# Kernel tuning notes

Measured on AMD Instinct MI355X. Metric: run time of the kernel, lower is better.

The kernel has to match this reference:

```python
import jax, jax.numpy as jnp
import numpy as np

D_MODEL = 256
D_STATE = 16
D_CONV = 4
DT_RANK = 16  # ceil(d_model/16)


def _silu(v):
    return v * jax.nn.sigmoid(v)


def _mamba(x, in_w, cw, cb, xp_w, dt_w, dt_b, A_log, Dp, out_w):
    """One Mamba head (d_inner == d_model since expand=1). x: (B, L, D)."""
    B, L, D = x.shape
    xz = x @ in_w.T                       # (B, L, 2D)
    xc, z = jnp.split(xz, 2, axis=-1)
    # causal depthwise conv1d, kernel D_CONV
    xpad = jnp.pad(xc, ((0, 0), (D_CONV - 1, 0), (0, 0)))
    conv = cb + sum(xpad[:, k:k + L, :] * cw[:, k] for k in range(D_CONV))
    xc = _silu(conv)
    dbl = xc @ xp_w.T                     # (B, L, dt_rank + 2N)
    dt_r = dbl[..., :DT_RANK]
    Bm = dbl[..., DT_RANK:DT_RANK + D_STATE]      # (B, L, N)
    Cm = dbl[..., DT_RANK + D_STATE:]             # (B, L, N)
    dt = jax.nn.softplus(dt_r @ dt_w.T + dt_b)    # (B, L, D)
    A = -jnp.exp(A_log)                            # (D, N)
    dA = jnp.exp(dt[..., None] * A)                # (B, L, D, N)
    dBx = (dt * xc)[..., None] * Bm[:, :, None, :] # (B, L, D, N)

    def step(h, inp):
        a, b = inp
        h = a * h + b
        return h, h

    h0 = jnp.zeros((B, D, D_STATE), x.dtype)
    _, hs = jax.lax.scan(step, h0, (jnp.moveaxis(dA, 1, 0), jnp.moveaxis(dBx, 1, 0)))
    y = jnp.einsum('lbdn,bln->bld', hs, Cm) + Dp * xc
    y = y * _silu(z)
    return y @ out_w.T


def setup_inputs() -> dict:
    key = jax.random.key(0)
    ks = jax.random.split(key, 8)
    D, N, R = D_MODEL, D_STATE, DT_RANK
    B, H, W = 4, 32, 32
    s = 0.02
    x = jax.random.normal(ks[0], (B, D, H, W), jnp.float32)
    in_proj_w = jax.random.normal(ks[1], (4, 2 * D, D), jnp.float32) * s
    conv_w = jax.random.normal(ks[2], (4, D, D_CONV), jnp.float32) * 0.1
    conv_b = jax.random.normal(ks[3], (4, D), jnp.float32) * 0.02
    x_proj_w = jax.random.normal(ks[4], (4, R + 2 * N, D), jnp.float32) * s
    dt_w = jax.random.normal(ks[5], (4, D, R), jnp.float32) * s
    dt_b = jax.random.normal(ks[6], (4, D), jnp.float32) * 0.02
    A_log = jnp.tile(jnp.log(jnp.arange(1, N + 1, dtype=jnp.float32)), (4, D, 1))
    D_skip = jnp.ones((4, D), jnp.float32)
    out_proj_w = jax.random.normal(ks[7], (4, D, D), jnp.float32) * s
    scale_mod = jnp.ones((1,), jnp.float32) * 0.25
    return {"x": x, "in_proj_w": in_proj_w, "conv_w": conv_w, "conv_b": conv_b,
            "x_proj_w": x_proj_w, "dt_w": dt_w, "dt_b": dt_b, "A_log": A_log,
            "D_skip": D_skip, "out_proj_w": out_proj_w, "scale_mod": scale_mod}


def reference(x, in_proj_w, conv_w, conv_b, x_proj_w, dt_w, dt_b, A_log, D_skip, out_proj_w, scale_mod):
    B, C, H, W = x.shape
    x_flat = x.transpose(0, 2, 3, 1).reshape(B, H * W, C)       # row-major scan order
    x_v = x_flat.reshape(B, H, W, C).transpose(0, 2, 1, 3).reshape(B, H * W, C)  # column-major
    inp4 = jnp.stack([x_flat, x_flat[:, ::-1], x_v, x_v[:, ::-1]])  # (4, B, L, C)
    outs = jax.vmap(_mamba)(inp4, in_proj_w, conv_w, conv_b, x_proj_w,
                            dt_w, dt_b, A_log, D_skip, out_proj_w)
    o0 = outs[0]
    o1 = outs[1][:, ::-1]
    o2 = outs[2].reshape(B, W, H, C).transpose(0, 2, 1, 3).reshape(B, H * W, C)
    o3 = outs[3][:, ::-1].reshape(B, W, H, C).transpose(0, 2, 1, 3).reshape(B, H * W, C)
    return (o0 + o1 + o2 + o3) / 4 * scale_mod
```

## Files before the change

### kernel.cpp

```cpp
#include <hip/hip_runtime.h>
#include <cstddef>

#define NDIR 4
#define NB 4
#define DM 256
#define NS 16
#define LL 1024
#define TCH 32
#define NCHUNK 32

typedef __attribute__((ext_vector_type(8))) short bf16x8;
typedef __attribute__((ext_vector_type(4))) float f32x4;

__device__ __forceinline__ float silu_f(float v) { return v / (1.0f + __expf(-v)); }
__device__ __forceinline__ float softplus_f(float v) {
    return fmaxf(v, 0.0f) + __logf(1.0f + __expf(-fabsf(v)));
}

__device__ __forceinline__ short bf16_hi(float v, float& vh) {
    unsigned u = __float_as_uint(v);
    unsigned r = (u + 0x7FFFu + ((u >> 16) & 1u)) & 0xFFFF0000u;
    vh = __uint_as_float(r);
    return (short)(r >> 16);
}
__device__ __forceinline__ short bf16_rn(float v) {
    unsigned u = __float_as_uint(v);
    return (short)((u + 0x7FFFu + ((u >> 16) & 1u)) >> 16);
}
__device__ __forceinline__ float bf16_to_f(short s) {
    return __uint_as_float(((unsigned)(unsigned short)s) << 16);
}

__device__ __forceinline__ int lmap(int dir, int l) {
    int lt = (dir & 2) ? (((l & 31) << 5) | (l >> 5)) : l;
    return (dir & 1) ? (1023 - lt) : lt;
}

__global__ __launch_bounds__(256) void k0w_prep(const float* __restrict__ x,
                                                const float* __restrict__ in_w,
                                                const float* __restrict__ xp_w,
                                                const float* __restrict__ out_w,
                                                short* __restrict__ Ah,
                                                short* __restrict__ Al,
                                                short* __restrict__ wh,
                                                short* __restrict__ wl) {
    int bid = blockIdx.x;
    int tid = threadIdx.x;
    if (bid < 1024) {
        int b  = bid & 3;
        int c0 = ((bid >> 2) & 7) << 5;
        int hh = (bid >> 5) & 31;
        __shared__ float T[32][33];
        int w  = tid & 31;
        int cl = tid >> 5;
#pragma unroll
        for (int it = 0; it < 4; ++it) {
            int c = cl + (it << 3);
            T[c][w] = x[(((size_t)(b << 8) + c0 + c) << 10) + (hh << 5) + w];
        }
        __syncthreads();
        int co = tid & 31;
        int wl_ = tid >> 5;
#pragma unroll
        for (int it = 0; it < 4; ++it) {
            int wo = wl_ + (it << 3);
            float v = T[co][wo];
            float vh;
            short hs = bf16_hi(v, vh);
            short ls = bf16_rn(v - vh);
            size_t idx = (((size_t)(b << 10) + (hh << 5) + wo) << 8) + c0 + co;
            Ah[idx] = hs;
            Al[idx] = ls;
        }
    } else {
        int t = ((bid - 1024) << 8) + tid;
        const float* src;
        size_t e;
        if (t < 131072)      { src = in_w  + ((size_t)t << 2);            e = (size_t)t << 2; }
        else if (t < 143360) { src = xp_w  + ((size_t)(t - 131072) << 2); e = 524288 + ((size_t)(t - 131072) << 2); }
        else                 { src = out_w + ((size_t)(t - 143360) << 2); e = 573440 + ((size_t)(t - 143360) << 2); }
        float4 v = *(const float4*)src;
        short4 H, L;
        float vh;
        H.x = bf16_hi(v.x, vh); L.x = bf16_rn(v.x - vh);
        H.y = bf16_hi(v.y, vh); L.y = bf16_rn(v.y - vh);
        H.z = bf16_hi(v.z, vh); L.z = bf16_rn(v.z - vh);
        H.w = bf16_hi(v.w, vh); L.w = bf16_rn(v.w - vh);
        *(short4*)(wh + e) = H;
        *(short4*)(wl + e) = L;
    }
}

__global__ __launch_bounds__(256, 2) void k1_mfma(const short* __restrict__ Ah,
                                                  const short* __restrict__ Al,
                                                  const short* __restrict__ Bh,
                                                  const short* __restrict__ Bl,
                                                  float* __restrict__ xzc,
                                                  float* __restrict__ xzz) {
    __shared__ short sAh[8192], sAl[8192], sBh[8192], sBl[8192];
    int mt = blockIdx.x, nt = blockIdx.y;
    int tid = threadIdx.x;
    int wv = tid >> 6, lane = tid & 63;
    int wm = wv >> 1, wn = wv & 1;
    int lrow = lane & 15, lk = lane >> 4;
    f32x4 acc[4][4] = {};
    int sr[4], sg[4], soff[4];
#pragma unroll
    for (int i = 0; i < 4; ++i) {
        int slot = (i << 8) + tid;
        sr[i] = slot >> 3; sg[i] = slot & 7;
        soff[i] = (sr[i] << 6) + ((sg[i] ^ (sr[i] & 7)) << 3);
    }
    bf16x8 vah[4], val_[4], vbh[4], vbl[4];
#define K1_LOAD(KK) do { \
    int k0_ = (KK) << 6; \
    _Pragma("unroll") \
    for (int i = 0; i < 4; ++i) { \
        size_t ao = (size_t)((mt << 7) + sr[i]) * 256 + k0_ + (sg[i] << 3); \
        size_t bo = (size_t)((nt << 7) + sr[i]) * 256 + k0_ + (sg[i] << 3); \
        vah[i]  = *(const bf16x8*)(Ah + ao); \
        val_[i] = *(const bf16x8*)(Al + ao); \
        vbh[i]  = *(const bf16x8*)(Bh + bo); \
        vbl[i]  = *(const bf16x8*)(Bl + bo); \
    } } while (0)
    K1_LOAD(0);
    for (int kk = 0; kk < 4; ++kk) {
        if (kk) __syncthreads();
#pragma unroll
        for (int i = 0; i < 4; ++i) {
            *(bf16x8*)&sAh[soff[i]] = vah[i];
            *(bf16x8*)&sAl[soff[i]] = val_[i];
            *(bf16x8*)&sBh[soff[i]] = vbh[i];
            *(bf16x8*)&sBl[soff[i]] = vbl[i];
        }
        __syncthreads();
        if (kk < 3) K1_LOAD(kk + 1);
#pragma unroll
        for (int kh = 0; kh < 2; ++kh) {
            int g = (kh << 2) + lk;
            bf16x8 ah[4], al[4], bh[4], bl[4];
#pragma unroll
            for (int m = 0; m < 4; ++m) {
                int r = (wm << 6) + (m << 4) + lrow;
                int off = (r << 6) + ((g ^ (r & 7)) << 3);
                ah[m] = *(const bf16x8*)&sAh[off];
                al[m] = *(const bf16x8*)&sAl[off];
            }
#pragma unroll
            for (int n = 0; n < 4; ++n) {
                int r = (wn << 6) + (n << 4) + lrow;
                int off = (r << 6) + ((g ^ (r & 7)) << 3);
                bh[n] = *(const bf16x8*)&sBh[off];
                bl[n] = *(const bf16x8*)&sBl[off];
            }
#pragma unroll
            for (int m = 0; m < 4; ++m)
#pragma unroll
                for (int n = 0; n < 4; ++n) {
                    acc[m][n] = __builtin_amdgcn_mfma_f32_16x16x32_bf16(ah[m], bh[n], acc[m][n], 0, 0, 0);
                    acc[m][n] = __builtin_amdgcn_mfma_f32_16x16x32_bf16(ah[m], bl[n], acc[m][n], 0, 0, 0);
                    acc[m][n] = __builtin_amdgcn_mfma_f32_16x16x32_bf16(al[m], bh[n], acc[m][n], 0, 0, 0);
                }
        }
    }
#undef K1_LOAD
#pragma unroll
    for (int n = 0; n < 4; ++n) {
        int gcol = (nt << 7) + (wn << 6) + (n << 4) + lrow;
        int dir = gcol >> 9, j = gcol & 511;
        float* dst = (j < 256) ? xzc : xzz;
        int jj = j & 255;
#pragma unroll
        for (int m = 0; m < 4; ++m) {
            int grow0 = (mt << 7) + (wm << 6) + (m << 4) + (lk << 2);
#pragma unroll
            for (int r = 0; r < 4; ++r) {
                int grow = grow0 + r;
                int b = grow >> 10, l = grow & 1023;
                int lo_ = lmap(dir, l);
                dst[((((size_t)((dir << 2) + b) << 10) + lo_) << 8) + jj] = acc[m][n][r];
            }
        }
    }
}

__global__ __launch_bounds__(256, 3) void k2_mega(const float* __restrict__ xzc,
                                                  const float* __restrict__ conv_w,
                                                  const float* __restrict__ conv_b,
                                                  const short* __restrict__ Bh,
                                                  const short* __restrict__ Bl,
                                                  const float* __restrict__ dt_w,
                                                  const float* __restrict__ dt_b,
                                                  const float* __restrict__ Dsk,
                                                  float* __restrict__ dbl,
                                                  float* __restrict__ ylocal,
                                                  float* __restrict__ hend,
                                                  float* __restrict__ Dend,
                                                  float* __restrict__ Dpre) {
    int bx   = blockIdx.x;
    int dirb = bx >> 5;
    int tile = bx & 31;
    int dir  = dirb >> 2;
    int tid  = threadIdx.x;
    __shared__ short xth[TCH * 256], xtl[TCH * 256];
    __shared__ float sdbl[TCH * 48];
    int base_row = (dirb << 10) + (tile << 5);

    {
        int qc = tid & 63;
        int c4 = qc << 2;
        float wch[4][4];
#pragma unroll
        for (int i = 0; i < 4; ++i) {
            float4 wv = *(const float4*)(conv_w + (((size_t)(dir << 8) + c4 + i) << 2));
            wch[i][0] = wv.x; wch[i][1] = wv.y; wch[i][2] = wv.z; wch[i][3] = wv.w;
        }
        float4 bias4 = *(const float4*)(conv_b + (dir << 8) + c4);
#pragma unroll
        for (int it = 0; it < 8; ++it) {
            int tok_l = (tid >> 6) + (it << 2);
            int lpos  = (tile << 5) + tok_l;
            float4 acc = bias4;
#pragma unroll
            for (int k = 0; k < 4; ++k) {
                int lk = lpos + k - 3;
                if (lk >= 0) {
                    float4 v = *(const float4*)(xzc + (((size_t)(dirb << 10) + lk) << 8) + c4);
                    acc.x += v.x * wch[0][k];
                    acc.y += v.y * wch[1][k];
                    acc.z += v.z * wch[2][k];
                    acc.w += v.w * wch[3][k];
                }
            }
            float o0 = silu_f(acc.x), o1 = silu_f(acc.y), o2 = silu_f(acc.z), o3 = silu_f(acc.w);
            short4 H, L;
            float vh;
            H.x = bf16_hi(o0, vh); L.x = bf16_rn(o0 - vh);
            H.y = bf16_hi(o1, vh); L.y = bf16_rn(o1 - vh);
            H.z = bf16_hi(o2, vh); L.z = bf16_rn(o2 - vh);
            H.w = bf16_hi(o3, vh); L.w = bf16_rn(o3 - vh);
            int gs = qc >> 1;
            int off = (tok_l << 8) + ((gs ^ (tok_l & 7)) << 3) + ((qc & 1) << 2);
            *(short4*)&xth[off] = H;
            *(short4*)&xtl[off] = L;
        }
    }
    __syncthreads();

    {
        int wv = tid >> 6, lane = tid & 63;
        int lrow = lane & 15, lk = lane >> 4;
        int m = wv & 1, nh = wv >> 1;
        f32x4 acc2[2] = {};
#pragma unroll
        for (int kk = 0; kk < 4; ++kk) {
#pragma unroll
            for (int kh = 0; kh < 2; ++kh) {
                int g = (kh << 2) + lk;
                int gs_abs = (kk << 3) + g;
                int ra = (m << 4) + lrow;
                int aoff = (ra << 8) + ((gs_abs ^ (ra & 7)) << 3);
                bf16x8 ah = *(const bf16x8*)&xth[aoff];
                bf16x8 al = *(const bf16x8*)&xtl[aoff];
#pragma unroll
                for (int ntile = 0; ntile < 2; ++ntile) {
                    int rb = (((nh << 1) + ntile) << 4) + lrow;
                    int rbc = rb < 48 ? rb : 47;
                    size_t bo = ((size_t)dir * 48 + rbc) * 256 + (kk << 6) + (g << 3);
                    bf16x8 bh = *(const bf16x8*)(Bh + bo);
                    bf16x8 bl = *(const bf16x8*)(Bl + bo);
                    acc2[ntile] = __builtin_amdgcn_mfma_f32_16x16x32_bf16(ah, bh, acc2[ntile], 0, 0, 0);
                    acc2[ntile] = __builtin_amdgcn_mfma_f32_16x16x32_bf16(ah, bl, acc2[ntile], 0, 0, 0);
                    acc2[ntile] = __builtin_amdgcn_mfma_f32_16x16x32_bf16(al, bh, acc2[ntile], 0, 0, 0);
                }
            }
        }
#pragma unroll
        for (int ntile = 0; ntile < 2; ++ntile) {
            int col = (((nh << 1) + ntile) << 4) + lrow;
            if (col < 48) {
#pragma unroll
                for (int r = 0; r < 4; ++r) {
                    int row_l = (m << 4) + (lk << 2) + r;
                    float v = acc2[ntile][r];
                    sdbl[row_l * 48 + col] = v;
                    dbl[(size_t)(base_row + row_l) * 48 + col] = v;
                }
            }
        }
    }
    __syncthreads();

    {
        int d = tid;
        float dtw[16];
        {
            const float4* wp = (const float4*)(dt_w + (((size_t)(dir << 8) + d) << 4));
            float4 w0 = wp[0], w1 = wp[1], w2 = wp[2], w3 = wp[3];
            dtw[0]=w0.x; dtw[1]=w0.y; dtw[2]=w0.z; dtw[3]=w0.w;
            dtw[4]=w1.x; dtw[5]=w1.y; dtw[6]=w1.z; dtw[7]=w1.w;
            dtw[8]=w2.x; dtw[9]=w2.y; dtw[10]=w2.z; dtw[11]=w2.w;
            dtw[12]=w3.x; dtw[13]=w3.y; dtw[14]=w3.z; dtw[15]=w3.w;
        }
        float bias = dt_b[(dir << 8) + d];
        float Dp   = Dsk[(dir << 8) + d];
        float h[16];
#pragma unroll
        for (int n = 0; n < 16; ++n) h[n] = 0.f;
        float D = 0.f;
        int chidx = (dirb << 5) + tile;
#pragma unroll 2
        for (int s = 0; s < TCH; ++s) {
            const float* row = &sdbl[s * 48];
            float4 q0 = *(const float4*)(row + 0);
            float4 q1 = *(const float4*)(row + 4);
            float4 q2 = *(const float4*)(row + 8);
            float4 q3 = *(const float4*)(row + 12);
            float d0 = q0.x*dtw[0] + q0.y*dtw[1] + q0.z*dtw[2] + q0.w*dtw[3];
            float d1 = q1.x*dtw[4] + q1.y*dtw[5] + q1.z*dtw[6] + q1.w*dtw[7];
            float d2 = q2.x*dtw[8] + q2.y*dtw[9] + q2.z*dtw[10] + q2.w*dtw[11];
            float d3 = q3.x*dtw[12] + q3.y*dtw[13] + q3.z*dtw[14] + q3.w*dtw[15];
            float dtv = softplus_f(bias + ((d0 + d1) + (d2 + d3)));
            D += dtv;
            if (s == 15) Dpre[(((size_t)chidx << 1) | 1) * 256 + d] = D;
            int toff = (s << 8) + (((d >> 3) ^ (s & 7)) << 3) + (d & 7);
            float txc = bf16_to_f(xth[toff]) + bf16_to_f(xtl[toff]);
            float r1 = __expf(-dtv);
            float r2 = r1*r1, r4 = r2*r2, r8 = r4*r4;
            float r3 = r2*r1, r5 = r4*r1, r6 = r4*r2, r7 = r4*r3;
            float r9 = r8*r1, r10 = r8*r2, r11 = r8*r3, r12 = r8*r4;
            float r13 = r8*r5, r14 = r8*r6, r15 = r8*r7, r16 = r8*r8;
            float dtxc = dtv * txc;
            float4 B0 = *(const float4*)(row + 16);
            float4 B1 = *(const float4*)(row + 20);
            float4 B2 = *(const float4*)(row + 24);
            float4 B3 = *(const float4*)(row + 28);
            float4 C0 = *(const float4*)(row + 32);
            float4 C1 = *(const float4*)(row + 36);
            float4 C2 = *(const float4*)(row + 40);
            float4 C3 = *(const float4*)(row + 44);
            float y0, y1, y2, y3;
            h[0]  = fmaf(r1,  h[0],  dtxc*B0.x); y0 = h[0]*C0.x;
            h[1]  = fmaf(r2,  h[1],  dtxc*B0.y); y1 = h[1]*C0.y;
            h[2]  = fmaf(r3,  h[2],  dtxc*B0.z); y2 = h[2]*C0.z;
            h[3]  = fmaf(r4,  h[3],  dtxc*B0.w); y3 = h[3]*C0.w;
            h[4]  = fmaf(r5,  h[4],  dtxc*B1.x); y0 = fmaf(h[4],  C1.x, y0);
            h[5]  = fmaf(r6,  h[5],  dtxc*B1.y); y1 = fmaf(h[5],  C1.y, y1);
            h[6]  = fmaf(r7,  h[6],  dtxc*B1.z); y2 = fmaf(h[6],  C1.z, y2);
            h[7]  = fmaf(r8,  h[7],  dtxc*B1.w); y3 = fmaf(h[7],  C1.w, y3);
            h[8]  = fmaf(r9,  h[8],  dtxc*B2.x); y0 = fmaf(h[8],  C2.x, y0);
            h[9]  = fmaf(r10, h[9],  dtxc*B2.y); y1 = fmaf(h[9],  C2.y, y1);
            h[10] = fmaf(r11, h[10], dtxc*B2.z); y2 = fmaf(h[10], C2.z, y2);
            h[11] = fmaf(r12, h[11], dtxc*B2.w); y3 = fmaf(h[11], C2.w, y3);
            h[12] = fmaf(r13, h[12], dtxc*B3.x); y0 = fmaf(h[12], C3.x, y0);
            h[13] = fmaf(r14, h[13], dtxc*B3.y); y1 = fmaf(h[13], C3.y, y1);
            h[14] = fmaf(r15, h[14], dtxc*B3.z); y2 = fmaf(h[14], C3.z, y2);
            h[15] = fmaf(r16, h[15], dtxc*B3.w); y3 = fmaf(h[15], C3.w, y3);
            float ysum = (y0 + y1) + (y2 + y3);
            ylocal[(size_t)(base_row + s) * 256 + d] = fmaf(Dp, txc, ysum);
        }
        size_t cb = (size_t)chidx << 4;
#pragma unroll
        for (int n = 0; n < 16; ++n)
            hend[(cb + n) * 256 + d] = h[n];
        Dend[(size_t)chidx * 256 + d] = D;
    }
}

__global__ __launch_bounds__(256) void k3b_combine(const float* __restrict__ Dend,
                                                   float* __restrict__ hweb) {
    int dirb = blockIdx.x >> 4;
    int n    = blockIdx.x & 15;
    int d    = threadIdx.x;
    float fn = -(float)(n + 1);
    size_t hbase = (((size_t)(dirb << 9)) + n) * 256 + d;
    size_t dbase = ((size_t)(dirb << 5)) * 256 + d;
    float h = 0.f;
    for (int g = 0; g < 2; ++g) {
        float De[16], he[16];
#pragma unroll
        for (int i = 0; i < 16; ++i) {
            int ch = (g << 4) + i;
            De[i] = Dend[dbase + (size_t)ch * 256];
            he[i] = hweb[hbase + (size_t)ch * 4096];
        }
#pragma unroll
        for (int i = 0; i < 16; ++i) {
            int ch = (g << 4) + i;
            float ap = __expf(fn * De[i]);
            hweb[hbase + (size_t)ch * 4096] = h;
            h = ap * h + he[i];
        }
    }
}

__global__ __launch_bounds__(256, 8) void k3c_finish(const float* __restrict__ ylocal,
                                                     const float* __restrict__ dbl,
                                                     const float* __restrict__ xzz,
                                                     const float* __restrict__ hweb,
                                                     const float* __restrict__ Dpre,
                                                     const float* __restrict__ dt_w,
                                                     const float* __restrict__ dt_b,
                                                     short* __restrict__ y_h,
                                                     short* __restrict__ y_l) {
    int bx   = blockIdx.x;
    int dirb = bx >> 6;
    int ch   = (bx >> 1) & 31;
    int sub  = bx & 1;
    int dir  = dirb >> 2;
    int b    = dirb & 3;
    int d    = threadIdx.x;
    __shared__ float shin[16 * 256];
    __shared__ float sdt[256];
    __shared__ float sC[256];
    int chidx = (dirb << 5) + ch;
    int base_row = (dirb << 10) + (ch << 5) + (sub << 4);
    {
        int s = d >> 4, j = d & 15;
        sdt[d] = dbl[(size_t)(base_row + s) * 48 + j];
        sC[d]  = dbl[(size_t)(base_row + s) * 48 + 32 + j];
    }
    size_t cb = (size_t)chidx << 4;
#pragma unroll
    for (int n = 0; n < 16; ++n)
        shin[(n << 8) + d] = hweb[(cb + n) * 256 + d];
    float dtw[16];
    {
        const float4* wp = (const float4*)(dt_w + (((size_t)(dir << 8) + d) << 4));
        float4 w0 = wp[0], w1 = wp[1], w2 = wp[2], w3 = wp[3];
        dtw[0]=w0.x; dtw[1]=w0.y; dtw[2]=w0.z; dtw[3]=w0.w;
        dtw[4]=w1.x; dtw[5]=w1.y; dtw[6]=w1.z; dtw[7]=w1.w;
        dtw[8]=w2.x; dtw[9]=w2.y; dtw[10]=w2.z; dtw[11]=w2.w;
        dtw[12]=w3.x; dtw[13]=w3.y; dtw[14]=w3.z; dtw[15]=w3.w;
    }
    float bias = dt_b[(dir << 8) + d];
    float D = sub ? Dpre[(((size_t)chidx << 1) | 1) * 256 + d] : 0.f;
    __syncthreads();
#pragma unroll 2
    for (int half = 0; half < 2; ++half) {
        float tyl[8], tz[8];
#pragma unroll
        for (int i = 0; i < 8; ++i) {
            size_t row = (size_t)(base_row + (half << 3) + i);
            tyl[i] = ylocal[row * 256 + d];
            tz[i]  = xzz[row * 256 + d];
        }
#pragma unroll
        for (int i = 0; i < 8; ++i) {
            int s = (half << 3) + i;
            const float* row = &sdt[s * 16];
            float4 q0 = *(const float4*)(row + 0);
            float4 q1 = *(const float4*)(row + 4);
            float4 q2 = *(const float4*)(row + 8);
            float4 q3 = *(const float4*)(row + 12);
            float d0 = q0.x*dtw[0] + q0.y*dtw[1] + q0.z*dtw[2] + q0.w*dtw[3];
            float d1 = q1.x*dtw[4] + q1.y*dtw[5] + q1.z*dtw[6] + q1.w*dtw[7];
            float d2 = q2.x*dtw[8] + q2.y*dtw[9] + q2.z*dtw[10] + q2.w*dtw[11];
            float d3 = q3.x*dtw[12] + q3.y*dtw[13] + q3.z*dtw[14] + q3.w*dtw[15];
            float dtv = softplus_f(bias + ((d0 + d1) + (d2 + d3)));
            D += dtv;
            float r1 = __expf(-D);
            const float* crow = &sC[s * 16];
            float p = r1;
            float y0 = (p * shin[d]) * crow[0];
            float y1, y2, y3;
            p *= r1; y1 = (p * shin[(1 << 8) + d]) * crow[1];
            p *= r1; y2 = (p * shin[(2 << 8) + d]) * crow[2];
            p *= r1; y3 = (p * shin[(3 << 8) + d]) * crow[3];
            p *= r1; y0 = fmaf(p * shin[(4 << 8) + d],  crow[4],  y0);
            p *= r1; y1 = fmaf(p * shin[(5 << 8) + d],  crow[5],  y1);
            p *= r1; y2 = fmaf(p * shin[(6 << 8) + d],  crow[6],  y2);
            p *= r1; y3 = fmaf(p * shin[(7 << 8) + d],  crow[7],  y3);
            p *= r1; y0 = fmaf(p * shin[(8 << 8) + d],  crow[8],  y0);
            p *= r1; y1 = fmaf(p * shin[(9 << 8) + d],  crow[9],  y1);
            p *= r1; y2 = fmaf(p * shin[(10 << 8) + d], crow[10], y2);
            p *= r1; y3 = fmaf(p * shin[(11 << 8) + d], crow[11], y3);
            p *= r1; y0 = fmaf(p * shin[(12 << 8) + d], crow[12], y0);
            p *= r1; y1 = fmaf(p * shin[(13 << 8) + d], crow[13], y1);
            p *= r1; y2 = fmaf(p * shin[(14 << 8) + d], crow[14], y2);
            p *= r1; y3 = fmaf(p * shin[(15 << 8) + d], crow[15], y3);
            float y = tyl[i] + ((y0 + y1) + (y2 + y3));
            y *= silu_f(tz[i]);
            float vh;
            short hs = bf16_hi(y, vh);
            short ls = bf16_rn(y - vh);
            int lc = lmap(dir, (ch << 5) + (sub << 4) + s);
            size_t yrow = (((size_t)(dir << 2) + b) << 10) + lc;
            y_h[yrow * 256 + d] = hs;
            y_l[yrow * 256 + d] = ls;
        }
    }
}

__global__ __launch_bounds__(256, 2) void k4_mfma(const short* __restrict__ Ah,
                                                  const short* __restrict__ Al,
                                                  const short* __restrict__ Bh,
                                                  const short* __restrict__ Bl,
                                                  float* __restrict__ part) {
    __shared__ short sAh[8192], sAl[8192], sBh[8192], sBl[8192];
    int mt = blockIdx.x, nt = blockIdx.y, dir = blockIdx.z;
    int tid = threadIdx.x;
    int wv = tid >> 6, lane = tid & 63;
    int wm = wv >> 1, wn = wv & 1;
    int lrow = lane & 15, lk = lane >> 4;
    f32x4 acc[4][4] = {};
    int sr[4], sg[4], soff[4];
#pragma unroll
    for (int i = 0; i < 4; ++i) {
        int slot = (i << 8) + tid;
        sr[i] = slot >> 3; sg[i] = slot & 7;
        soff[i] = (sr[i] << 6) + ((sg[i] ^ (sr[i] & 7)) << 3);
    }
    bf16x8 vah[4], val_[4], vbh[4], vbl[4];
#define K4_LOAD(KK) do { \
    int k0_ = (KK) << 6; \
    _Pragma("unroll") \
    for (int i = 0; i < 4; ++i) { \
        size_t ao = ((size_t)(dir << 12) + (mt << 7) + sr[i]) * 256 + k0_ + (sg[i] << 3); \
        size_t bo = ((size_t)(dir << 8) + (nt << 7) + sr[i]) * 256 + k0_ + (sg[i] << 3); \
        vah[i]  = *(const bf16x8*)(Ah + ao); \
        val_[i] = *(const bf16x8*)(Al + ao); \
        vbh[i]  = *(const bf16x8*)(Bh + bo); \
        vbl[i]  = *(const bf16x8*)(Bl + bo); \
    } } while (0)
    K4_LOAD(0);
    for (int kk = 0; kk < 4; ++kk) {
        if (kk) __syncthreads();
#pragma unroll
        for (int i = 0; i < 4; ++i) {
            *(bf16x8*)&sAh[soff[i]] = vah[i];
            *(bf16x8*)&sAl[soff[i]] = val_[i];
            *(bf16x8*)&sBh[soff[i]] = vbh[i];
            *(bf16x8*)&sBl[soff[i]] = vbl[i];
        }
        __syncthreads();
        if (kk < 3) K4_LOAD(kk + 1);
#pragma unroll
        for (int kh = 0; kh < 2; ++kh) {
            int g = (kh << 2) + lk;
            bf16x8 ah[4], al[4], bh[4], bl[4];
#pragma unroll
            for (int m = 0; m < 4; ++m) {
                int r = (wm << 6) + (m << 4) + lrow;
                int off = (r << 6) + ((g ^ (r & 7)) << 3);
                ah[m] = *(const bf16x8*)&sAh[off];
                al[m] = *(const bf16x8*)&sAl[off];
            }
#pragma unroll
            for (int n = 0; n < 4; ++n) {
                int r = (wn << 6) + (n << 4) + lrow;
                int off = (r << 6) + ((g ^ (r & 7)) << 3);
                bh[n] = *(const bf16x8*)&sBh[off];
                bl[n] = *(const bf16x8*)&sBl[off];
            }
#pragma unroll
            for (int m = 0; m < 4; ++m)
#pragma unroll
                for (int n = 0; n < 4; ++n) {
                    acc[m][n] = __builtin_amdgcn_mfma_f32_16x16x32_bf16(ah[m], bh[n], acc[m][n], 0, 0, 0);
                    acc[m][n] = __builtin_amdgcn_mfma_f32_16x16x32_bf16(ah[m], bl[n], acc[m][n], 0, 0, 0);
                    acc[m][n] = __builtin_amdgcn_mfma_f32_16x16x32_bf16(al[m], bh[n], acc[m][n], 0, 0, 0);
                }
        }
    }
#undef K4_LOAD
    float* pd = part + ((size_t)dir << 20);
#pragma unroll
    for (int n = 0; n < 4; ++n) {
        int gcol = (nt << 7) + (wn << 6) + (n << 4) + lrow;
#pragma unroll
        for (int m = 0; m < 4; ++m) {
            int grow0 = (mt << 7) + (wm << 6) + (m << 4) + (lk << 2);
#pragma unroll
            for (int r = 0; r < 4; ++r)
                pd[(size_t)(grow0 + r) * 256 + gcol] = acc[m][n][r];
        }
    }
}

__global__ __launch_bounds__(256) void k4b_reduce(const float* __restrict__ part,
                                                  const float* __restrict__ smod,
                                                  float* __restrict__ out) {
    size_t o = ((size_t)(blockIdx.x << 8) + threadIdx.x) << 2;
    const size_t S = (size_t)4096 * 256;
    float4 a = *(const float4*)(part + o);
    float4 b = *(const float4*)(part + S + o);
    float4 c = *(const float4*)(part + 2 * S + o);
    float4 d = *(const float4*)(part + 3 * S + o);
    float sc = smod[0] * 0.25f;
    float4 r;
    r.x = (a.x + b.x + c.x + d.x) * sc;
    r.y = (a.y + b.y + c.y + d.y) * sc;
    r.z = (a.z + b.z + c.z + d.z) * sc;
    r.w = (a.w + b.w + c.w + d.w) * sc;
    *(float4*)(out + o) = r;
}

extern "C" void kernel_launch(void* const* d_in, const int* in_sizes, int n_in,
                              void* d_out, int out_size, void* d_ws, size_t ws_size,
                              hipStream_t stream) {
    const float* x     = (const float*)d_in[0];
    const float* in_w  = (const float*)d_in[1];
    const float* cw    = (const float*)d_in[2];
    const float* cb    = (const float*)d_in[3];
    const float* xp_w  = (const float*)d_in[4];
    const float* dt_w  = (const float*)d_in[5];
    const float* dt_b  = (const float*)d_in[6];
    const float* Dsk   = (const float*)d_in[8];
    const float* out_w = (const float*)d_in[9];
    const float* smod  = (const float*)d_in[10];

    float* ws = (float*)d_ws;
    float* xzc    = ws;
    float* xzz    = xzc + 4194304;
    float* ylocal = xzz + 4194304;
    float* dbl    = ylocal + 4194304;
    float* hweb   = dbl + 786432;
    short* inpA_h = (short*)(hweb + 2097152);
    short* inpA_l = inpA_h + 1048576;
    short* y_h    = inpA_l + 1048576;
    short* y_l    = y_h + 4194304;
    short* w_h    = y_l + 4194304;
    short* w_l    = w_h + 835584;
    short* inw_h  = w_h,          * inw_l  = w_l;
    short* xpw_h  = w_h + 524288, * xpw_l  = w_l + 524288;
    short* outw_h = w_h + 573440, * outw_l = w_l + 573440;
    float* Dend   = (float*)inpA_h;
    float* Dpre   = Dend + 131072;
    float* part4  = xzc;

    k0w_prep<<<1840, 256, 0, stream>>>(x, in_w, xp_w, out_w, inpA_h, inpA_l, w_h, w_l);
    k1_mfma<<<dim3(32, 16), 256, 0, stream>>>(inpA_h, inpA_l, inw_h, inw_l, xzc, xzz);
    k2_mega<<<512, 256, 0, stream>>>(xzc, cw, cb, xpw_h, xpw_l, dt_w, dt_b, Dsk,
                                     dbl, ylocal, hweb, Dend, Dpre);
    k3b_combine<<<256, 256, 0, stream>>>(Dend, hweb);
    k3c_finish<<<1024, 256, 0, stream>>>(ylocal, dbl, xzz, hweb, Dpre, dt_w, dt_b,
                                         y_h, y_l);
    k4_mfma<<<dim3(32, 2, 4), 256, 0, stream>>>(y_h, y_l, outw_h, outw_l, part4);
    k4b_reduce<<<1024, 256, 0, stream>>>(part4, smod, (float*)d_out);
}
```

Measured before the change: 101.7 us.

## Halve scan chunk length and fuse out-projection with direction reduction

```diff
diff --git a/kernel.cpp b/kernel.cpp
--- a/kernel.cpp
+++ b/kernel.cpp
@@ -6,8 +6,8 @@
 #define DM 256
 #define NS 16
 #define LL 1024
-#define TCH 32
-#define NCHUNK 32
+#define TCH 16
+#define NCHUNK 64
 
 typedef __attribute__((ext_vector_type(8))) short bf16x8;
 typedef __attribute__((ext_vector_type(4))) float f32x4;
@@ -184,7 +184,7 @@
     }
 }
 
-__global__ __launch_bounds__(256, 3) void k2_mega(const float* __restrict__ xzc,
+__global__ __launch_bounds__(256, 4) void k2_mega(const float* __restrict__ xzc,
                                                   const float* __restrict__ conv_w,
                                                   const float* __restrict__ conv_b,
                                                   const short* __restrict__ Bh,
@@ -198,13 +198,13 @@
                                                   float* __restrict__ Dend,
                                                   float* __restrict__ Dpre) {
     int bx   = blockIdx.x;
-    int dirb = bx >> 5;
-    int tile = bx & 31;
+    int dirb = bx >> 6;
+    int tile = bx & 63;
     int dir  = dirb >> 2;
     int tid  = threadIdx.x;
     __shared__ short xth[TCH * 256], xtl[TCH * 256];
     __shared__ float sdbl[TCH * 48];
-    int base_row = (dirb << 10) + (tile << 5);
+    int base_row = (dirb << 10) + (tile << 4);
 
     {
         int qc = tid & 63;
@@ -217,9 +217,9 @@
         }
         float4 bias4 = *(const float4*)(conv_b + (dir << 8) + c4);
 #pragma unroll
-        for (int it = 0; it < 8; ++it) {
+        for (int it = 0; it < 4; ++it) {
             int tok_l = (tid >> 6) + (it << 2);
-            int lpos  = (tile << 5) + tok_l;
+            int lpos  = (tile << 4) + tok_l;
             float4 acc = bias4;
 #pragma unroll
             for (int k = 0; k < 4; ++k) {
@@ -250,42 +250,33 @@
     {
         int wv = tid >> 6, lane = tid & 63;
         int lrow = lane & 15, lk = lane >> 4;
-        int m = wv & 1, nh = wv >> 1;
-        f32x4 acc2[2] = {};
-#pragma unroll
-        for (int kk = 0; kk < 4; ++kk) {
-#pragma unroll
-            for (int kh = 0; kh < 2; ++kh) {
-                int g = (kh << 2) + lk;
-                int gs_abs = (kk << 3) + g;
-                int ra = (m << 4) + lrow;
-                int aoff = (ra << 8) + ((gs_abs ^ (ra & 7)) << 3);
-                bf16x8 ah = *(const bf16x8*)&xth[aoff];
-                bf16x8 al = *(const bf16x8*)&xtl[aoff];
-#pragma unroll
-                for (int ntile = 0; ntile < 2; ++ntile) {
-                    int rb = (((nh << 1) + ntile) << 4) + lrow;
-                    int rbc = rb < 48 ? rb : 47;
-                    size_t bo = ((size_t)dir * 48 + rbc) * 256 + (kk << 6) + (g << 3);
+        if (wv < 3) {
+            f32x4 acc2 = {};
+#pragma unroll
+            for (int kk = 0; kk < 4; ++kk) {
+#pragma unroll
+                for (int kh = 0; kh < 2; ++kh) {
+                    int g = (kh << 2) + lk;
+                    int gs_abs = (kk << 3) + g;
+                    int aoff = (lrow << 8) + ((gs_abs ^ (lrow & 7)) << 3);
+                    bf16x8 ah = *(const bf16x8*)&xth[aoff];
+                    bf16x8 al = *(const bf16x8*)&xtl[aoff];
+                    int rb = (wv << 4) + lrow;
+                    size_t bo = ((size_t)dir * 48 + rb) * 256 + (kk << 6) + (g << 3);
                     bf16x8 bh = *(const bf16x8*)(Bh + bo);
                     bf16x8 bl = *(const bf16x8*)(Bl + bo);
-                    acc2[ntile] = __builtin_amdgcn_mfma_f32_16x16x32_bf16(ah, bh, acc2[ntile], 0, 0, 0);
-                    acc2[ntile] = __builtin_amdgcn_mfma_f32_16x16x32_bf16(ah, bl, acc2[ntile], 0, 0, 0);
-                    acc2[ntile] = __builtin_amdgcn_mfma_f32_16x16x32_bf16(al, bh, acc2[ntile], 0, 0, 0);
+                    acc2 = __builtin_amdgcn_mfma_f32_16x16x32_bf16(ah, bh, acc2, 0, 0, 0);
+                    acc2 = __builtin_amdgcn_mfma_f32_16x16x32_bf16(ah, bl, acc2, 0, 0, 0);
+                    acc2 = __builtin_amdgcn_mfma_f32_16x16x32_bf16(al, bh, acc2, 0, 0, 0);
                 }
             }
-        }
-#pragma unroll
-        for (int ntile = 0; ntile < 2; ++ntile) {
-            int col = (((nh << 1) + ntile) << 4) + lrow;
-            if (col < 48) {
-#pragma unroll
-                for (int r = 0; r < 4; ++r) {
-                    int row_l = (m << 4) + (lk << 2) + r;
-                    float v = acc2[ntile][r];
-                    sdbl[row_l * 48 + col] = v;
-                    dbl[(size_t)(base_row + row_l) * 48 + col] = v;
-                }
+            int col = (wv << 4) + lrow;
+#pragma unroll
+            for (int r = 0; r < 4; ++r) {
+                int row_l = (lk << 2) + r;
+                float v = acc2[r];
+                sdbl[row_l * 48 + col] = v;
+                dbl[(size_t)(base_row + row_l) * 48 + col] = v;
             }
         }
     }
@@ -308,8 +299,8 @@
 #pragma unroll
         for (int n = 0; n < 16; ++n) h[n] = 0.f;
         float D = 0.f;
-        int chidx = (dirb << 5) + tile;
-#pragma unroll 2
+        int chidx = (dirb << 6) + tile;
+#pragma unroll
         for (int s = 0; s < TCH; ++s) {
             const float* row = &sdbl[s * 48];
             float4 q0 = *(const float4*)(row + 0);
@@ -322,7 +313,7 @@
             float d3 = q3.x*dtw[12] + q3.y*dtw[13] + q3.z*dtw[14] + q3.w*dtw[15];
             float dtv = softplus_f(bias + ((d0 + d1) + (d2 + d3)));
             D += dtv;
-            if (s == 15) Dpre[(((size_t)chidx << 1) | 1) * 256 + d] = D;
+            if (s == 7) Dpre[(size_t)chidx * 256 + d] = D;
             int toff = (s << 8) + (((d >> 3) ^ (s & 7)) << 3) + (d & 7);
             float txc = bf16_to_f(xth[toff]) + bf16_to_f(xtl[toff]);
             float r1 = __expf(-dtv);
@@ -373,10 +364,10 @@
     int n    = blockIdx.x & 15;
     int d    = threadIdx.x;
     float fn = -(float)(n + 1);
-    size_t hbase = (((size_t)(dirb << 9)) + n) * 256 + d;
-    size_t dbase = ((size_t)(dirb << 5)) * 256 + d;
+    size_t hbase = ((size_t)(dirb << 10) + n) * 256 + d;
+    size_t dbase = ((size_t)(dirb << 6)) * 256 + d;
     float h = 0.f;
-    for (int g = 0; g < 2; ++g) {
+    for (int g = 0; g < 4; ++g) {
         float De[16], he[16];
 #pragma unroll
         for (int i = 0; i < 16; ++i) {
@@ -404,21 +395,22 @@
                                                      short* __restrict__ y_h,
                                                      short* __restrict__ y_l) {
     int bx   = blockIdx.x;
-    int dirb = bx >> 6;
-    int ch   = (bx >> 1) & 31;
+    int dirb = bx >> 7;
+    int ch   = (bx >> 1) & 63;
     int sub  = bx & 1;
     int dir  = dirb >> 2;
     int b    = dirb & 3;
     int d    = threadIdx.x;
     __shared__ float shin[16 * 256];
-    __shared__ float sdt[256];
-    __shared__ float sC[256];
-    int chidx = (dirb << 5) + ch;
-    int base_row = (dirb << 10) + (ch << 5) + (sub << 4);
+    __shared__ float sdt[128];
+    __shared__ float sC[128];
+    int chidx = (dirb << 6) + ch;
+    int base_row = (dirb << 10) + (ch << 4) + (sub << 3);
     {
-        int s = d >> 4, j = d & 15;
-        sdt[d] = dbl[(size_t)(base_row + s) * 48 + j];
-        sC[d]  = dbl[(size_t)(base_row + s) * 48 + 32 + j];
+        int s = (d >> 4) & 7, j = d & 15;
+        float v = dbl[(size_t)(base_row + s) * 48 + ((d & 128) ? 32 : 0) + j];
+        if (d < 128) sdt[(s << 4) + j] = v;
+        else         sC[(s << 4) + j]  = v;
     }
     size_t cb = (size_t)chidx << 4;
 #pragma unroll
@@ -434,166 +426,139 @@
         dtw[12]=w3.x; dtw[13]=w3.y; dtw[14]=w3.z; dtw[15]=w3.w;
     }
     float bias = dt_b[(dir << 8) + d];
-    float D = sub ? Dpre[(((size_t)chidx << 1) | 1) * 256 + d] : 0.f;
+    float D = sub ? Dpre[(size_t)chidx * 256 + d] : 0.f;
     __syncthreads();
-#pragma unroll 2
-    for (int half = 0; half < 2; ++half) {
-        float tyl[8], tz[8];
-#pragma unroll
-        for (int i = 0; i < 8; ++i) {
-            size_t row = (size_t)(base_row + (half << 3) + i);
-            tyl[i] = ylocal[row * 256 + d];
-            tz[i]  = xzz[row * 256 + d];
-        }
-#pragma unroll
-        for (int i = 0; i < 8; ++i) {
-            int s = (half << 3) + i;
-            const float* row = &sdt[s * 16];
-            float4 q0 = *(const float4*)(row + 0);
-            float4 q1 = *(const float4*)(row + 4);
-            float4 q2 = *(const float4*)(row + 8);
-            float4 q3 = *(const float4*)(row + 12);
-            float d0 = q0.x*dtw[0] + q0.y*dtw[1] + q0.z*dtw[2] + q0.w*dtw[3];
-            float d1 = q1.x*dtw[4] + q1.y*dtw[5] + q1.z*dtw[6] + q1.w*dtw[7];
-            float d2 = q2.x*dtw[8] + q2.y*dtw[9] + q2.z*dtw[10] + q2.w*dtw[11];
-            float d3 = q3.x*dtw[12] + q3.y*dtw[13] + q3.z*dtw[14] + q3.w*dtw[15];
-            float dtv = softplus_f(bias + ((d0 + d1) + (d2 + d3)));
-            D += dtv;
-            float r1 = __expf(-D);
-            const float* crow = &sC[s * 16];
-            float p = r1;
-            float y0 = (p * shin[d]) * crow[0];
-            float y1, y2, y3;
-            p *= r1; y1 = (p * shin[(1 << 8) + d]) * crow[1];
-            p *= r1; y2 = (p * shin[(2 << 8) + d]) * crow[2];
-            p *= r1; y3 = (p * shin[(3 << 8) + d]) * crow[3];
-            p *= r1; y0 = fmaf(p * shin[(4 << 8) + d],  crow[4],  y0);
-            p *= r1; y1 = fmaf(p * shin[(5 << 8) + d],  crow[5],  y1);
-            p *= r1; y2 = fmaf(p * shin[(6 << 8) + d],  crow[6],  y2);
-            p *= r1; y3 = fmaf(p * shin[(7 << 8) + d],  crow[7],  y3);
-            p *= r1; y0 = fmaf(p * shin[(8 << 8) + d],  crow[8],  y0);
-            p *= r1; y1 = fmaf(p * shin[(9 << 8) + d],  crow[9],  y1);
-            p *= r1; y2 = fmaf(p * shin[(10 << 8) + d], crow[10], y2);
-            p *= r1; y3 = fmaf(p * shin[(11 << 8) + d], crow[11], y3);
-            p *= r1; y0 = fmaf(p * shin[(12 << 8) + d], crow[12], y0);
-            p *= r1; y1 = fmaf(p * shin[(13 << 8) + d], crow[13], y1);
-            p *= r1; y2 = fmaf(p * shin[(14 << 8) + d], crow[14], y2);
-            p *= r1; y3 = fmaf(p * shin[(15 << 8) + d], crow[15], y3);
-            float y = tyl[i] + ((y0 + y1) + (y2 + y3));
-            y *= silu_f(tz[i]);
-            float vh;
-            short hs = bf16_hi(y, vh);
-            short ls = bf16_rn(y - vh);
-            int lc = lmap(dir, (ch << 5) + (sub << 4) + s);
-            size_t yrow = (((size_t)(dir << 2) + b) << 10) + lc;
-            y_h[yrow * 256 + d] = hs;
-            y_l[yrow * 256 + d] = ls;
-        }
-    }
-}
-
-__global__ __launch_bounds__(256, 2) void k4_mfma(const short* __restrict__ Ah,
-                                                  const short* __restrict__ Al,
-                                                  const short* __restrict__ Bh,
-                                                  const short* __restrict__ Bl,
-                                                  float* __restrict__ part) {
-    __shared__ short sAh[8192], sAl[8192], sBh[8192], sBl[8192];
-    int mt = blockIdx.x, nt = blockIdx.y, dir = blockIdx.z;
+    float tyl[8], tz[8];
+#pragma unroll
+    for (int i = 0; i < 8; ++i) {
+        size_t row = (size_t)(base_row + i);
+        tyl[i] = ylocal[row * 256 + d];
+        tz[i]  = xzz[row * 256 + d];
+    }
+#pragma unroll
+    for (int s = 0; s < 8; ++s) {
+        const float* row = &sdt[s * 16];
+        float4 q0 = *(const float4*)(row + 0);
+        float4 q1 = *(const float4*)(row + 4);
+        float4 q2 = *(const float4*)(row + 8);
+        float4 q3 = *(const float4*)(row + 12);
+        float d0 = q0.x*dtw[0] + q0.y*dtw[1] + q0.z*dtw[2] + q0.w*dtw[3];
+        float d1 = q1.x*dtw[4] + q1.y*dtw[5] + q1.z*dtw[6] + q1.w*dtw[7];
+        float d2 = q2.x*dtw[8] + q2.y*dtw[9] + q2.z*dtw[10] + q2.w*dtw[11];
+        float d3 = q3.x*dtw[12] + q3.y*dtw[13] + q3.z*dtw[14] + q3.w*dtw[15];
+        float dtv = softplus_f(bias + ((d0 + d1) + (d2 + d3)));
+        D += dtv;
+        float r1 = __expf(-D);
+        const float* crow = &sC[s * 16];
+        float p = r1;
+        float y0 = (p * shin[d]) * crow[0];
+        float y1, y2, y3;
+        p *= r1; y1 = (p * shin[(1 << 8) + d]) * crow[1];
+        p *= r1; y2 = (p * shin[(2 << 8) + d]) * crow[2];
+        p *= r1; y3 = (p * shin[(3 << 8) + d]) * crow[3];
+        p *= r1; y0 = fmaf(p * shin[(4 << 8) + d],  crow[4],  y0);
+        p *= r1; y1 = fmaf(p * shin[(5 << 8) + d],  crow[5],  y1);
+        p *= r1; y2 = fmaf(p * shin[(6 << 8) + d],  crow[6],  y2);
+        p *= r1; y3 = fmaf(p * shin[(7 << 8) + d],  crow[7],  y3);
+        p *= r1; y0 = fmaf(p * shin[(8 << 8) + d],  crow[8],  y0);
+        p *= r1; y1 = fmaf(p * shin[(9 << 8) + d],  crow[9],  y1);
+        p *= r1; y2 = fmaf(p * shin[(10 << 8) + d], crow[10], y2);
+        p *= r1; y3 = fmaf(p * shin[(11 << 8) + d], crow[11], y3);
+        p *= r1; y0 = fmaf(p * shin[(12 << 8) + d], crow[12], y0);
+        p *= r1; y1 = fmaf(p * shin[(13 << 8) + d], crow[13], y1);
+        p *= r1; y2 = fmaf(p * shin[(14 << 8) + d], crow[14], y2);
+        p *= r1; y3 = fmaf(p * shin[(15 << 8) + d], crow[15], y3);
+        float y = tyl[s] + ((y0 + y1) + (y2 + y3));
+        y *= silu_f(tz[s]);
+        float vh;
+        short hs = bf16_hi(y, vh);
+        short ls = bf16_rn(y - vh);
+        int lc = lmap(dir, (ch << 4) + (sub << 3) + s);
+        size_t yrow = (((size_t)(dir << 2) + b) << 10) + lc;
+        y_h[yrow * 256 + d] = hs;
+        y_l[yrow * 256 + d] = ls;
+    }
+}
+
+__global__ __launch_bounds__(256, 2) void k4_fused(const short* __restrict__ Ah,
+                                                   const short* __restrict__ Al,
+                                                   const short* __restrict__ Bh,
+                                                   const short* __restrict__ Bl,
+                                                   const float* __restrict__ smod,
+                                                   float* __restrict__ out) {
+    __shared__ short sAh[2048], sAl[2048], sBh[4096], sBl[4096];
+    int mt = blockIdx.x, nt = blockIdx.y;
     int tid = threadIdx.x;
     int wv = tid >> 6, lane = tid & 63;
-    int wm = wv >> 1, wn = wv & 1;
+    int wn = wv;
     int lrow = lane & 15, lk = lane >> 4;
-    f32x4 acc[4][4] = {};
-    int sr[4], sg[4], soff[4];
-#pragma unroll
-    for (int i = 0; i < 4; ++i) {
+    f32x4 acc[2] = {};
+    int ra_s = tid >> 3, ga_s = tid & 7;
+    int aoff_s = (ra_s << 6) + ((ga_s ^ (ra_s & 7)) << 3);
+    int rb_s[2], gb_s[2], boff_s[2];
+#pragma unroll
+    for (int i = 0; i < 2; ++i) {
         int slot = (i << 8) + tid;
-        sr[i] = slot >> 3; sg[i] = slot & 7;
-        soff[i] = (sr[i] << 6) + ((sg[i] ^ (sr[i] & 7)) << 3);
-    }
-    bf16x8 vah[4], val_[4], vbh[4], vbl[4];
-#define K4_LOAD(KK) do { \
-    int k0_ = (KK) << 6; \
+        rb_s[i] = slot >> 3; gb_s[i] = slot & 7;
+        boff_s[i] = (rb_s[i] << 6) + ((gb_s[i] ^ (rb_s[i] & 7)) << 3);
+    }
+    bf16x8 vah, val_, vbh[2], vbl[2];
+#define K4_LOAD(ST) do { \
+    int dir_ = (ST) >> 2, kk_ = (ST) & 3; \
+    size_t ao = ((size_t)(dir_ << 12) + (mt << 5) + ra_s) * 256 + (kk_ << 6) + (ga_s << 3); \
+    vah  = *(const bf16x8*)(Ah + ao); \
+    val_ = *(const bf16x8*)(Al + ao); \
     _Pragma("unroll") \
-    for (int i = 0; i < 4; ++i) { \
-        size_t ao = ((size_t)(dir << 12) + (mt << 7) + sr[i]) * 256 + k0_ + (sg[i] << 3); \
-        size_t bo = ((size_t)(dir << 8) + (nt << 7) + sr[i]) * 256 + k0_ + (sg[i] << 3); \
-        vah[i]  = *(const bf16x8*)(Ah + ao); \
-        val_[i] = *(const bf16x8*)(Al + ao); \
-        vbh[i]  = *(const bf16x8*)(Bh + bo); \
-        vbl[i]  = *(const bf16x8*)(Bl + bo); \
+    for (int i = 0; i < 2; ++i) { \
+        size_t bo = ((size_t)(dir_ << 8) + (nt << 6) + rb_s[i]) * 256 + (kk_ << 6) + (gb_s[i] << 3); \
+        vbh[i] = *(const bf16x8*)(Bh + bo); \
+        vbl[i] = *(const bf16x8*)(Bl + bo); \
     } } while (0)
     K4_LOAD(0);
-    for (int kk = 0; kk < 4; ++kk) {
-        if (kk) __syncthreads();
-#pragma unroll
-        for (int i = 0; i < 4; ++i) {
-            *(bf16x8*)&sAh[soff[i]] = vah[i];
-            *(bf16x8*)&sAl[soff[i]] = val_[i];
-            *(bf16x8*)&sBh[soff[i]] = vbh[i];
-            *(bf16x8*)&sBl[soff[i]] = vbl[i];
+    for (int step = 0; step < 16; ++step) {
+        if (step) __syncthreads();
+        *(bf16x8*)&sAh[aoff_s] = vah;
+        *(bf16x8*)&sAl[aoff_s] = val_;
+#pragma unroll
+        for (int i = 0; i < 2; ++i) {
+            *(bf16x8*)&sBh[boff_s[i]] = vbh[i];
+            *(bf16x8*)&sBl[boff_s[i]] = vbl[i];
         }
         __syncthreads();
-        if (kk < 3) K4_LOAD(kk + 1);
+        if (step < 15) K4_LOAD(step + 1);
 #pragma unroll
         for (int kh = 0; kh < 2; ++kh) {
             int g = (kh << 2) + lk;
-            bf16x8 ah[4], al[4], bh[4], bl[4];
-#pragma unroll
-            for (int m = 0; m < 4; ++m) {
-                int r = (wm << 6) + (m << 4) + lrow;
+            bf16x8 ahm[2], alm[2];
+#pragma unroll
+            for (int m = 0; m < 2; ++m) {
+                int r = (m << 4) + lrow;
                 int off = (r << 6) + ((g ^ (r & 7)) << 3);
-                ah[m] = *(const bf16x8*)&sAh[off];
-                al[m] = *(const bf16x8*)&sAl[off];
-            }
-#pragma unroll
-            for (int n = 0; n < 4; ++n) {
-                int r = (wn << 6) + (n << 4) + lrow;
-                int off = (r << 6) + ((g ^ (r & 7)) << 3);
-                bh[n] = *(const bf16x8*)&sBh[off];
-                bl[n] = *(const bf16x8*)&sBl[off];
-            }
-#pragma unroll
-            for (int m = 0; m < 4; ++m)
-#pragma unroll
-                for (int n = 0; n < 4; ++n) {
-                    acc[m][n] = __builtin_amdgcn_mfma_f32_16x16x32_bf16(ah[m], bh[n], acc[m][n], 0, 0, 0);
-                    acc[m][n] = __builtin_amdgcn_mfma_f32_16x16x32_bf16(ah[m], bl[n], acc[m][n], 0, 0, 0);
-                    acc[m][n] = __builtin_amdgcn_mfma_f32_16x16x32_bf16(al[m], bh[n], acc[m][n], 0, 0, 0);
-                }
+                ahm[m] = *(const bf16x8*)&sAh[off];
+                alm[m] = *(const bf16x8*)&sAl[off];
+            }
+            int rbw = (wn << 4) + lrow;
+            int offb = (rbw << 6) + ((g ^ (rbw & 7)) << 3);
+            bf16x8 bh = *(const bf16x8*)&sBh[offb];
+            bf16x8 bl = *(const bf16x8*)&sBl[offb];
+#pragma unroll
+            for (int m = 0; m < 2; ++m) {
+                acc[m] = __builtin_amdgcn_mfma_f32_16x16x32_bf16(ahm[m], bh, acc[m], 0, 0, 0);
+                acc[m] = __builtin_amdgcn_mfma_f32_16x16x32_bf16(ahm[m], bl, acc[m], 0, 0, 0);
+                acc[m] = __builtin_amdgcn_mfma_f32_16x16x32_bf16(alm[m], bh, acc[m], 0, 0, 0);
+            }
         }
     }
 #undef K4_LOAD
-    float* pd = part + ((size_t)dir << 20);
-#pragma unroll
-    for (int n = 0; n < 4; ++n) {
-        int gcol = (nt << 7) + (wn << 6) + (n << 4) + lrow;
-#pragma unroll
-        for (int m = 0; m < 4; ++m) {
-            int grow0 = (mt << 7) + (wm << 6) + (m << 4) + (lk << 2);
-#pragma unroll
-            for (int r = 0; r < 4; ++r)
-                pd[(size_t)(grow0 + r) * 256 + gcol] = acc[m][n][r];
-        }
-    }
-}
-
-__global__ __launch_bounds__(256) void k4b_reduce(const float* __restrict__ part,
-                                                  const float* __restrict__ smod,
-                                                  float* __restrict__ out) {
-    size_t o = ((size_t)(blockIdx.x << 8) + threadIdx.x) << 2;
-    const size_t S = (size_t)4096 * 256;
-    float4 a = *(const float4*)(part + o);
-    float4 b = *(const float4*)(part + S + o);
-    float4 c = *(const float4*)(part + 2 * S + o);
-    float4 d = *(const float4*)(part + 3 * S + o);
     float sc = smod[0] * 0.25f;
-    float4 r;
-    r.x = (a.x + b.x + c.x + d.x) * sc;
-    r.y = (a.y + b.y + c.y + d.y) * sc;
-    r.z = (a.z + b.z + c.z + d.z) * sc;
-    r.w = (a.w + b.w + c.w + d.w) * sc;
-    *(float4*)(out + o) = r;
+    int gcol = (nt << 6) + (wn << 4) + lrow;
+#pragma unroll
+    for (int m = 0; m < 2; ++m) {
+        int grow0 = (mt << 5) + (m << 4) + (lk << 2);
+#pragma unroll
+        for (int r = 0; r < 4; ++r)
+            out[(size_t)(grow0 + r) * 256 + gcol] = acc[m][r] * sc;
+    }
 }
 
 extern "C" void kernel_launch(void* const* d_in, const int* in_sizes, int n_in,
@@ -616,7 +581,7 @@
     float* ylocal = xzz + 4194304;
     float* dbl    = ylocal + 4194304;
     float* hweb   = dbl + 786432;
-    short* inpA_h = (short*)(hweb + 2097152);
+    short* inpA_h = (short*)(hweb + 4194304);
     short* inpA_l = inpA_h + 1048576;
     short* y_h    = inpA_l + 1048576;
     short* y_l    = y_h + 4194304;
@@ -626,16 +591,15 @@
     short* xpw_h  = w_h + 524288, * xpw_l  = w_l + 524288;
     short* outw_h = w_h + 573440, * outw_l = w_l + 573440;
     float* Dend   = (float*)inpA_h;
-    float* Dpre   = Dend + 131072;
-    float* part4  = xzc;
+    float* Dpre   = (float*)inpA_l;
 
     k0w_prep<<<1840, 256, 0, stream>>>(x, in_w, xp_w, out_w, inpA_h, inpA_l, w_h, w_l);
     k1_mfma<<<dim3(32, 16), 256, 0, stream>>>(inpA_h, inpA_l, inw_h, inw_l, xzc, xzz);
-    k2_mega<<<512, 256, 0, stream>>>(xzc, cw, cb, xpw_h, xpw_l, dt_w, dt_b, Dsk,
-                                     dbl, ylocal, hweb, Dend, Dpre);
+    k2_mega<<<1024, 256, 0, stream>>>(xzc, cw, cb, xpw_h, xpw_l, dt_w, dt_b, Dsk,
+                                      dbl, ylocal, hweb, Dend, Dpre);
     k3b_combine<<<256, 256, 0, stream>>>(Dend, hweb);
-    k3c_finish<<<1024, 256, 0, stream>>>(ylocal, dbl, xzz, hweb, Dpre, dt_w, dt_b,
+    k3c_finish<<<2048, 256, 0, stream>>>(ylocal, dbl, xzz, hweb, Dpre, dt_w, dt_b,
                                          y_h, y_l);
-    k4_mfma<<<dim3(32, 2, 4), 256, 0, stream>>>(y_h, y_l, outw_h, outw_l, part4);
-    k4b_reduce<<<1024, 256, 0, stream>>>(part4, smod, (float*)d_out);
-}
+    k4_fused<<<dim3(128, 4), 256, 0, stream>>>(y_h, y_l, outw_h, outw_l, smod,
+                                               (float*)d_out);
+}
```

Result: faster. 90.50 us (-11.0%).
